# Kernel optimization log

Measured on AMD Instinct MI355X. Metric: run time of the kernel, lower is better.

The kernel has to match this reference:

```python
import jax, jax.numpy as jnp
import numpy as np
import math

D_MODEL = 768
H = 12
D_K = D_MODEL // H


def setup_inputs() -> dict:
    key = jax.random.key(0)
    ks = jax.random.split(key, 12)
    B, S = 2, 2048
    q = jax.random.normal(ks[0], (B, S, D_MODEL), dtype=jnp.float32)
    k = jax.random.normal(ks[1], (B, S, D_MODEL), dtype=jnp.float32)
    v = jax.random.normal(ks[2], (B, S, D_MODEL), dtype=jnp.float32)
    mask = jax.random.randint(ks[3], (1, 1, S, S), 0, 2, dtype=jnp.int32)
    scale = 1.0 / math.sqrt(D_MODEL)
    w_q = jax.random.normal(ks[4], (D_MODEL, D_MODEL), dtype=jnp.float32) * scale
    b_q = jnp.zeros((D_MODEL,), dtype=jnp.float32)
    w_k = jax.random.normal(ks[5], (D_MODEL, D_MODEL), dtype=jnp.float32) * scale
    b_k = jnp.zeros((D_MODEL,), dtype=jnp.float32)
    w_v = jax.random.normal(ks[6], (D_MODEL, D_MODEL), dtype=jnp.float32) * scale
    b_v = jnp.zeros((D_MODEL,), dtype=jnp.float32)
    w_o = jax.random.normal(ks[7], (D_MODEL, D_MODEL), dtype=jnp.float32) * scale
    b_o = jnp.zeros((D_MODEL,), dtype=jnp.float32)
    return {"q": q, "k": k, "v": v, "mask": mask,
            "w_q": w_q, "b_q": b_q, "w_k": w_k, "b_k": b_k,
            "w_v": w_v, "b_v": b_v, "w_o": w_o, "b_o": b_o}


def reference(q, k, v, mask, w_q, b_q, w_k, b_k, w_v, b_v, w_o, b_o):
    B, S, _ = q.shape
    # torch nn.Linear: y = x @ W^T + b
    qp = (q @ w_q.T + b_q).reshape(B, S, H, D_K).transpose(0, 2, 1, 3)  # [B,H,S,Dk]
    kp = (k @ w_k.T + b_k).reshape(B, S, H, D_K).transpose(0, 2, 1, 3)
    vp = (v @ w_v.T + b_v).reshape(B, S, H, D_K).transpose(0, 2, 1, 3)
    # full [B,H,S,S] score matrix (the memory-bound round-trip)
    scores = jnp.einsum('bhqd,bhkd->bhqk', qp, kp) / math.sqrt(D_K)
    scores = jnp.where(mask == 0, jnp.float32(-1e9), scores)
    attn = jax.nn.softmax(scores, axis=-1)
    x = jnp.einsum('bhqk,bhkd->bhqd', attn, vp)  # [B,H,S,Dk]
    x = x.transpose(0, 2, 1, 3).reshape(B, S, H * D_K)
    return x @ w_o.T + b_o
```

## Files before the change

kernel.cpp:

```cpp
#include <hip/hip_runtime.h>
#include <hip/hip_bf16.h>

typedef __attribute__((ext_vector_type(8))) __bf16 bf16x8;
typedef __attribute__((ext_vector_type(8))) short short8;
typedef __attribute__((ext_vector_type(4))) float f32x4;

#define LOG2E 1.44269504088896f
#define SCL (0.125f * 1.44269504088896f)

static __device__ __forceinline__ ushort f2bf(float f) {
  union { float f; unsigned u; } x; x.f = f;
  unsigned r = x.u + 0x7fffu + ((x.u >> 16) & 1u);
  return (ushort)(r >> 16);
}

static __device__ __forceinline__ unsigned cvt_pk_bf16(float a, float b) {
  unsigned r;
  asm("v_cvt_pk_bf16_f32 %0, %1, %2" : "=v"(r) : "v"(a), "v"(b));
  return r;
}

static __device__ __forceinline__ void gll16(const ushort* g, ushort* l) {
  __builtin_amdgcn_global_load_lds(
      (const __attribute__((address_space(1))) unsigned*)g,
      (__attribute__((address_space(3))) unsigned*)l, 16, 0, 0);
}

#define NQ 3145728u
#define NW 589824u
__global__ __launch_bounds__(256)
void cvt_all(const float* __restrict__ q, const float* __restrict__ k,
             const float* __restrict__ v,
             const float* __restrict__ wq, const float* __restrict__ wk,
             const float* __restrict__ wv, const float* __restrict__ wo,
             ushort* __restrict__ dst)
{
  size_t i = ((size_t)blockIdx.x * 256 + threadIdx.x) * 4;
  const float* src; size_t off;
  if (i < NQ)                { src = q;  off = i; }
  else if (i < 2u * NQ)      { src = k;  off = i - NQ; }
  else if (i < 3u * NQ)      { src = v;  off = i - 2u * NQ; }
  else {
    size_t j = i - 3u * NQ;
    if (j < NW)            { src = wq; off = j; }
    else if (j < 2u * NW)  { src = wk; off = j - NW; }
    else if (j < 3u * NW)  { src = wv; off = j - 2u * NW; }
    else                   { src = wo; off = j - 3u * NW; }
  }
  f32x4 x = *(const f32x4*)(src + off);
  uint2 o;
  o.x = cvt_pk_bf16(x[0], x[1]);
  o.y = cvt_pk_bf16(x[2], x[3]);
  *(uint2*)(dst + i) = o;
}

__global__ __launch_bounds__(256)
void mask_pack(const int* __restrict__ mask, unsigned long long* __restrict__ mb)
{
  size_t gw = (size_t)blockIdx.x * 4 + (threadIdx.x >> 6);
  int lane = threadIdx.x & 63;
  int mk = mask[gw * 64 + lane];
  unsigned long long bits = __ballot(mk != 0);
  if (lane == 0) mb[gw] = bits;
}

template<int MODE>
static __device__ __forceinline__ void gemm_core(const ushort* __restrict__ A,
                                                 const ushort* __restrict__ Wrow0,
                                                 const float* __restrict__ bias0,
                                                 void* __restrict__ outv,
                                                 int m0, int c0)
{
  constexpr int K = 768;
  constexpr int BK = 64;
  __shared__ ushort As[2][128 * BK];
  __shared__ ushort Bs[2][128 * BK];
  const int tid  = threadIdx.x;
  const int lane = tid & 63;
  const int wid  = tid >> 6;
  const int wr = (wid >> 1) * 64;
  const int wc = (wid & 1) * 64;

  f32x4 acc[4][4];
#pragma unroll
  for (int i = 0; i < 4; i++)
#pragma unroll
    for (int j = 0; j < 4; j++) acc[i][j] = f32x4{0.f, 0.f, 0.f, 0.f};

  const ushort* gA[4]; const ushort* gB[4];
  int loff[4];
#pragma unroll
  for (int s = 0; s < 4; s++) {
    int idx = tid + s * 256;
    int row = idx >> 3, col = (idx & 7) * 8;
    gA[s] = A     + (size_t)(m0 + row) * K + col;
    gB[s] = Wrow0 + (size_t)row * K + col;
    loff[s] = idx * 8;
  }

  const int fr  = lane & 15;
  const int kg8 = (lane >> 4) * 8;

#pragma unroll
  for (int s = 0; s < 4; s++) {
    gll16(gA[s], &As[0][loff[s]]);
    gll16(gB[s], &Bs[0][loff[s]]);
  }
  __syncthreads();

  int cur = 0;
  for (int t = 0; t < K / BK; t++) {
    if (t < K / BK - 1) {
      const int kt = (t + 1) * BK;
#pragma unroll
      for (int s = 0; s < 4; s++) {
        gll16(gA[s] + kt, &As[cur ^ 1][loff[s]]);
        gll16(gB[s] + kt, &Bs[cur ^ 1][loff[s]]);
      }
    }
    bf16x8 af[2][4], wf[2][4];
#pragma unroll
    for (int kk = 0; kk < 2; kk++) {
#pragma unroll
      for (int i = 0; i < 4; i++) af[kk][i] = *(const bf16x8*)&As[cur][(wr + i * 16 + fr) * BK + kk * 32 + kg8];
#pragma unroll
      for (int j = 0; j < 4; j++) wf[kk][j] = *(const bf16x8*)&Bs[cur][(wc + j * 16 + fr) * BK + kk * 32 + kg8];
    }
#pragma unroll
    for (int kk = 0; kk < 2; kk++)
#pragma unroll
      for (int i = 0; i < 4; i++)
#pragma unroll
        for (int j = 0; j < 4; j++)
          acc[i][j] = __builtin_amdgcn_mfma_f32_16x16x32_bf16(af[kk][i], wf[kk][j], acc[i][j], 0, 0, 0);
    __syncthreads();
    cur ^= 1;
  }

#pragma unroll
  for (int i = 0; i < 4; i++) {
#pragma unroll
    for (int j = 0; j < 4; j++) {
#pragma unroll
      for (int r = 0; r < 4; r++) {
        int m  = m0 + wr + i * 16 + (lane >> 4) * 4 + r;
        int lc = wc + j * 16 + fr;
        float val = acc[i][j][r] + bias0[lc];
        if (MODE == 0) {
          int nn = c0 + lc;
          int hh = nn >> 6, dk = nn & 63;
          ((ushort*)outv)[(((size_t)(m >> 11) * 12 + hh) * 2048 + (m & 2047)) * 64 + dk] = f2bf(val);
        } else {
          ((float*)outv)[(size_t)m * 768 + c0 + lc] = val;
        }
      }
    }
  }
}

__global__ __launch_bounds__(256)
void qkv_gemm2(const ushort* __restrict__ CV,
               const float* __restrict__ bq, const float* __restrict__ bk,
               const float* __restrict__ bv,
               ushort* __restrict__ Qp, ushort* __restrict__ Kp, ushort* __restrict__ Vp)
{
  const int m0 = blockIdx.x * 128;
  const int n0 = blockIdx.y * 128;
  const int proj = n0 / 768;
  const int c0 = n0 - proj * 768;
  const ushort* A  = CV + (size_t)proj * NQ;
  const ushort* Wc = CV + (size_t)3 * NQ;
  const float* bias = (proj == 0) ? bq : (proj == 1) ? bk : bv;
  ushort* O = (proj == 0) ? Qp : (proj == 1) ? Kp : Vp;
  gemm_core<0>(A, Wc + (size_t)n0 * 768, bias + c0, O, m0, c0);
}

__global__ __launch_bounds__(256)
void o_gemm2(const ushort* __restrict__ X, const ushort* __restrict__ Wo,
             const float* __restrict__ bo, float* __restrict__ out)
{
  const int m0 = blockIdx.x * 128;
  const int n0 = blockIdx.y * 128;
  gemm_core<1>(X, Wo + (size_t)n0 * 768, bo + n0, out, m0, n0);
}

__global__ __launch_bounds__(256, 3)
void attn_kernel(const ushort* __restrict__ Qp, const ushort* __restrict__ Kp,
                 const ushort* __restrict__ Vp,
                 const unsigned long long* __restrict__ mb,
                 ushort* __restrict__ X)
{
  constexpr int S = 2048;
  __shared__ ushort Ks[128][72];
  __shared__ ushort Vt[64][136];
  __shared__ ushort Ps[4][16][136];

  const int tid  = threadIdx.x;
  const int lane = tid & 63;
  const int w    = tid >> 6;
  const int bid  = blockIdx.x;
  const int bh = (bid & 7) + 8 * (bid >> 8);
  const int qb = (bid >> 3) & 31;
  const int b = bh / 12, h = bh % 12;

  const ushort* Qb = Qp + (size_t)bh * S * 64;
  const ushort* Kb = Kp + (size_t)bh * S * 64;
  const ushort* Vb = Vp + (size_t)bh * S * 64;

  const int q0  = qb * 64;
  const int fr  = lane & 15;
  const int g   = lane >> 4;
  const int kg8 = g * 8;
  const int qrow4 = q0 + w * 16 + g * 4;

  const int qrow = q0 + w * 16 + fr;
  bf16x8 qf0 = *(const bf16x8*)&Qb[(size_t)qrow * 64 + kg8];
  bf16x8 qf1 = *(const bf16x8*)&Qb[(size_t)qrow * 64 + 32 + kg8];

  float m_r[4] = {-1e9f, -1e9f, -1e9f, -1e9f};
  float l_r[4] = {0.f, 0.f, 0.f, 0.f};
  f32x4 accO[4];
#pragma unroll
  for (int ni = 0; ni < 4; ni++) accO[ni] = f32x4{0.f, 0.f, 0.f, 0.f};

  const int skey = tid >> 2;
  const int sc0  = (tid & 3) * 16;
  const uint4* mb4 = (const uint4*)mb;

  short8 kr0, kr1, kr2, kr3, vr0, vr1, vr2, vr3;
  {
    const ushort* kb = Kb + (size_t)skey * 64 + sc0;
    const ushort* vb = Vb + (size_t)skey * 64 + sc0;
    kr0 = *(const short8*)kb;          kr1 = *(const short8*)(kb + 8);
    kr2 = *(const short8*)(kb + 4096); kr3 = *(const short8*)(kb + 4104);
    vr0 = *(const short8*)vb;          vr1 = *(const short8*)(vb + 8);
    vr2 = *(const short8*)(vb + 4096); vr3 = *(const short8*)(vb + 4104);
  }

  for (int tt = 0; tt < 16; tt++) {
    __syncthreads();
    *(short8*)&Ks[skey][sc0]          = kr0;
    *(short8*)&Ks[skey][sc0 + 8]      = kr1;
    *(short8*)&Ks[64 + skey][sc0]     = kr2;
    *(short8*)&Ks[64 + skey][sc0 + 8] = kr3;
#pragma unroll
    for (int i = 0; i < 8; i++) {
      Vt[sc0 + i][skey]          = (ushort)vr0[i];
      Vt[sc0 + 8 + i][skey]      = (ushort)vr1[i];
      Vt[sc0 + i][64 + skey]     = (ushort)vr2[i];
      Vt[sc0 + 8 + i][64 + skey] = (ushort)vr3[i];
    }
    __syncthreads();

    uint4 mB[4];
#pragma unroll
    for (int r = 0; r < 4; r++)
      mB[r] = mb4[(size_t)(qrow4 + r) * 16 + tt];

    if (tt < 15) {
      const ushort* kb = Kb + (size_t)((tt + 1) * 128 + skey) * 64 + sc0;
      const ushort* vb = Vb + (size_t)((tt + 1) * 128 + skey) * 64 + sc0;
      kr0 = *(const short8*)kb;          kr1 = *(const short8*)(kb + 8);
      kr2 = *(const short8*)(kb + 4096); kr3 = *(const short8*)(kb + 4104);
      vr0 = *(const short8*)vb;          vr1 = *(const short8*)(vb + 8);
      vr2 = *(const short8*)(vb + 4096); vr3 = *(const short8*)(vb + 4104);
    }

    f32x4 sc8[8];
#pragma unroll
    for (int ni = 0; ni < 8; ni++) {
      bf16x8 kf0 = *(const bf16x8*)&Ks[ni * 16 + fr][kg8];
      bf16x8 kf1 = *(const bf16x8*)&Ks[ni * 16 + fr][32 + kg8];
      f32x4 c = {0.f, 0.f, 0.f, 0.f};
      c = __builtin_amdgcn_mfma_f32_16x16x32_bf16(qf0, kf0, c, 0, 0, 0);
      c = __builtin_amdgcn_mfma_f32_16x16x32_bf16(qf1, kf1, c, 0, 0, 0);
      sc8[ni] = c;
    }

#pragma unroll
    for (int r = 0; r < 4; r++) {
      float praw[8];
#pragma unroll
      for (int ni = 0; ni < 8; ni++) praw[ni] = sc8[ni][r] * SCL;
      float mx = fmaxf(fmaxf(fmaxf(praw[0], praw[1]), fmaxf(praw[2], praw[3])),
                       fmaxf(fmaxf(praw[4], praw[5]), fmaxf(praw[6], praw[7])));
      mx = fmaxf(mx, __shfl_xor(mx, 1));
      mx = fmaxf(mx, __shfl_xor(mx, 2));
      mx = fmaxf(mx, __shfl_xor(mx, 4));
      mx = fmaxf(mx, __shfl_xor(mx, 8));
      if (mx > m_r[r] + 11.5f) {
        float al = exp2f(m_r[r] - mx);
        m_r[r] = mx;
        l_r[r] *= al;
#pragma unroll
        for (int ni = 0; ni < 4; ni++) accO[ni][r] *= al;
      }
      const float mr = m_r[r];
      unsigned sx = mB[r].x >> fr, sy = mB[r].y >> fr,
               sz = mB[r].z >> fr, sw = mB[r].w >> fr;
      unsigned bits[8] = { sx & 1u, (sx >> 16) & 1u, sy & 1u, (sy >> 16) & 1u,
                           sz & 1u, (sz >> 16) & 1u, sw & 1u, (sw >> 16) & 1u };
      float e[8];
      float ls = 0.f;
#pragma unroll
      for (int ni = 0; ni < 8; ni++) {
        float t = exp2f(praw[ni] - mr);
        t = bits[ni] ? t : 0.f;
        e[ni] = t; ls += t;
      }
      ls += __shfl_xor(ls, 1);
      ls += __shfl_xor(ls, 2);
      ls += __shfl_xor(ls, 4);
      ls += __shfl_xor(ls, 8);
      l_r[r] += ls;
#pragma unroll
      for (int a = 0; a < 4; a++) {
        unsigned pk = cvt_pk_bf16(e[2 * a], e[2 * a + 1]);
        Ps[w][g * 4 + r][a * 32 + fr]      = (ushort)pk;
        Ps[w][g * 4 + r][a * 32 + 16 + fr] = (ushort)(pk >> 16);
      }
    }

#pragma unroll
    for (int ks = 0; ks < 4; ks++) {
      bf16x8 pf = *(const bf16x8*)&Ps[w][fr][ks * 32 + kg8];
#pragma unroll
      for (int ni = 0; ni < 4; ni++) {
        bf16x8 vf = *(const bf16x8*)&Vt[ni * 16 + fr][ks * 32 + kg8];
        accO[ni] = __builtin_amdgcn_mfma_f32_16x16x32_bf16(pf, vf, accO[ni], 0, 0, 0);
      }
    }
  }

  float inv[4];
#pragma unroll
  for (int r = 0; r < 4; r++) inv[r] = 1.f / l_r[r];
#pragma unroll
  for (int ni = 0; ni < 4; ni++) {
#pragma unroll
    for (int r = 0; r < 4; r++) {
      int qq = qrow4 + r;
      float o = accO[ni][r] * inv[r];
      X[((size_t)b * S + qq) * 768 + h * 64 + ni * 16 + fr] = f2bf(o);
    }
  }
}

extern "C" void kernel_launch(void* const* d_in, const int* in_sizes, int n_in,
                              void* d_out, int out_size, void* d_ws, size_t ws_size,
                              hipStream_t stream) {
  const float* q  = (const float*)d_in[0];
  const float* k  = (const float*)d_in[1];
  const float* v  = (const float*)d_in[2];
  const int* mask = (const int*)d_in[3];
  const float* wq = (const float*)d_in[4];
  const float* bq = (const float*)d_in[5];
  const float* wk = (const float*)d_in[6];
  const float* bk = (const float*)d_in[7];
  const float* wv = (const float*)d_in[8];
  const float* bv = (const float*)d_in[9];
  const float* wo = (const float*)d_in[10];
  const float* bo = (const float*)d_in[11];
  float* out = (float*)d_out;

  ushort* CV = (ushort*)d_ws;
  ushort* Qp = CV + (size_t)3 * NQ + (size_t)4 * NW;
  ushort* Kp = Qp + NQ;
  ushort* Vp = Kp + NQ;
  ushort* Xb = Vp + NQ;
  unsigned long long* mbuf = (unsigned long long*)CV;

  cvt_all<<<11520, 256, 0, stream>>>(q, k, v, wq, wk, wv, wo, CV);
  qkv_gemm2<<<dim3(32, 18), dim3(256), 0, stream>>>(CV, bq, bk, bv, Qp, Kp, Vp);
  mask_pack<<<16384, 256, 0, stream>>>(mask, mbuf);
  attn_kernel<<<768, 256, 0, stream>>>(Qp, Kp, Vp, mbuf, Xb);
  o_gemm2<<<dim3(32, 6), dim3(256), 0, stream>>>(Xb, CV + (size_t)3 * NQ + (size_t)3 * NW, bo, out);
}
```

Before: 266.1 us.

## Store V transposed from QKV GEMM and XOR-swizzle attention LDS tiles

The QKV projection now writes V in a [bh][dk][seq] transposed layout, so the attention kernel can load V^T tiles with vector loads and write them to LDS as 16-byte stores instead of scalar transposing writes. The K, V^T and P shared-memory tiles drop their padding and use an XOR swizzle on the column index to avoid bank conflicts. The aim is to cut LDS store instruction count and bank conflicts in the attention inner loop. In exchange, the GEMM epilogue for V writes with a strided, uncoalesced pattern, which may slow that kernel.

```diff
diff --git a/kernel.cpp b/kernel.cpp
--- a/kernel.cpp
+++ b/kernel.cpp
@@ -150,6 +150,11 @@
           int nn = c0 + lc;
           int hh = nn >> 6, dk = nn & 63;
           ((ushort*)outv)[(((size_t)(m >> 11) * 12 + hh) * 2048 + (m & 2047)) * 64 + dk] = f2bf(val);
+        } else if (MODE == 2) {
+          int nn = c0 + lc;
+          int hh = nn >> 6, dk = nn & 63;
+          int bh = (m >> 11) * 12 + hh;
+          ((ushort*)outv)[((size_t)bh * 64 + dk) * 2048 + (m & 2047)] = f2bf(val);
         } else {
           ((float*)outv)[(size_t)m * 768 + c0 + lc] = val;
         }
@@ -172,7 +177,10 @@
   const ushort* Wc = CV + (size_t)3 * NQ;
   const float* bias = (proj == 0) ? bq : (proj == 1) ? bk : bv;
   ushort* O = (proj == 0) ? Qp : (proj == 1) ? Kp : Vp;
-  gemm_core<0>(A, Wc + (size_t)n0 * 768, bias + c0, O, m0, c0);
+  if (proj == 2)
+    gemm_core<2>(A, Wc + (size_t)n0 * 768, bias + c0, O, m0, c0);
+  else
+    gemm_core<0>(A, Wc + (size_t)n0 * 768, bias + c0, O, m0, c0);
 }
 
 __global__ __launch_bounds__(256)
@@ -186,14 +194,14 @@
 
 __global__ __launch_bounds__(256, 3)
 void attn_kernel(const ushort* __restrict__ Qp, const ushort* __restrict__ Kp,
-                 const ushort* __restrict__ Vp,
+                 const ushort* __restrict__ VpT,
                  const unsigned long long* __restrict__ mb,
                  ushort* __restrict__ X)
 {
   constexpr int S = 2048;
-  __shared__ ushort Ks[128][72];
-  __shared__ ushort Vt[64][136];
-  __shared__ ushort Ps[4][16][136];
+  __shared__ ushort Ks[128][64];
+  __shared__ ushort Vt[64][128];
+  __shared__ ushort Ps[4][16][128];
 
   const int tid  = threadIdx.x;
   const int lane = tid & 63;
@@ -203,9 +211,9 @@
   const int qb = (bid >> 3) & 31;
   const int b = bh / 12, h = bh % 12;
 
-  const ushort* Qb = Qp + (size_t)bh * S * 64;
-  const ushort* Kb = Kp + (size_t)bh * S * 64;
-  const ushort* Vb = Vp + (size_t)bh * S * 64;
+  const ushort* Qb  = Qp  + (size_t)bh * S * 64;
+  const ushort* Kb  = Kp  + (size_t)bh * S * 64;
+  const ushort* gVt = VpT + (size_t)bh * 64 * S;
 
   const int q0  = qb * 64;
   const int fr  = lane & 15;
@@ -225,31 +233,35 @@
 
   const int skey = tid >> 2;
   const int sc0  = (tid & 3) * 16;
+  const int kxor = (skey & 7) << 3;
+  const int vd   = tid >> 4;
+  const int vkc  = (tid & 15) * 8;
+  const int vxor = (vd & 7) << 3;
+
   const uint4* mb4 = (const uint4*)mb;
 
   short8 kr0, kr1, kr2, kr3, vr0, vr1, vr2, vr3;
   {
     const ushort* kb = Kb + (size_t)skey * 64 + sc0;
-    const ushort* vb = Vb + (size_t)skey * 64 + sc0;
     kr0 = *(const short8*)kb;          kr1 = *(const short8*)(kb + 8);
     kr2 = *(const short8*)(kb + 4096); kr3 = *(const short8*)(kb + 4104);
-    vr0 = *(const short8*)vb;          vr1 = *(const short8*)(vb + 8);
-    vr2 = *(const short8*)(vb + 4096); vr3 = *(const short8*)(vb + 4104);
+    const ushort* vb = gVt + (size_t)vd * S + vkc;
+    vr0 = *(const short8*)vb;
+    vr1 = *(const short8*)(vb + 16 * S);
+    vr2 = *(const short8*)(vb + 32 * S);
+    vr3 = *(const short8*)(vb + 48 * S);
   }
 
   for (int tt = 0; tt < 16; tt++) {
     __syncthreads();
-    *(short8*)&Ks[skey][sc0]          = kr0;
-    *(short8*)&Ks[skey][sc0 + 8]      = kr1;
-    *(short8*)&Ks[64 + skey][sc0]     = kr2;
-    *(short8*)&Ks[64 + skey][sc0 + 8] = kr3;
-#pragma unroll
-    for (int i = 0; i < 8; i++) {
-      Vt[sc0 + i][skey]          = (ushort)vr0[i];
-      Vt[sc0 + 8 + i][skey]      = (ushort)vr1[i];
-      Vt[sc0 + i][64 + skey]     = (ushort)vr2[i];
-      Vt[sc0 + 8 + i][64 + skey] = (ushort)vr3[i];
-    }
+    *(short8*)&Ks[skey][sc0 ^ kxor]            = kr0;
+    *(short8*)&Ks[skey][(sc0 + 8) ^ kxor]      = kr1;
+    *(short8*)&Ks[64 + skey][sc0 ^ kxor]       = kr2;
+    *(short8*)&Ks[64 + skey][(sc0 + 8) ^ kxor] = kr3;
+    *(short8*)&Vt[vd][vkc ^ vxor]       = vr0;
+    *(short8*)&Vt[vd + 16][vkc ^ vxor]  = vr1;
+    *(short8*)&Vt[vd + 32][vkc ^ vxor]  = vr2;
+    *(short8*)&Vt[vd + 48][vkc ^ vxor]  = vr3;
     __syncthreads();
 
     uint4 mB[4];
@@ -259,18 +271,22 @@
 
     if (tt < 15) {
       const ushort* kb = Kb + (size_t)((tt + 1) * 128 + skey) * 64 + sc0;
-      const ushort* vb = Vb + (size_t)((tt + 1) * 128 + skey) * 64 + sc0;
       kr0 = *(const short8*)kb;          kr1 = *(const short8*)(kb + 8);
       kr2 = *(const short8*)(kb + 4096); kr3 = *(const short8*)(kb + 4104);
-      vr0 = *(const short8*)vb;          vr1 = *(const short8*)(vb + 8);
-      vr2 = *(const short8*)(vb + 4096); vr3 = *(const short8*)(vb + 4104);
+      const ushort* vb = gVt + (size_t)vd * S + (tt + 1) * 128 + vkc;
+      vr0 = *(const short8*)vb;
+      vr1 = *(const short8*)(vb + 16 * S);
+      vr2 = *(const short8*)(vb + 32 * S);
+      vr3 = *(const short8*)(vb + 48 * S);
     }
 
     f32x4 sc8[8];
 #pragma unroll
     for (int ni = 0; ni < 8; ni++) {
-      bf16x8 kf0 = *(const bf16x8*)&Ks[ni * 16 + fr][kg8];
-      bf16x8 kf1 = *(const bf16x8*)&Ks[ni * 16 + fr][32 + kg8];
+      const int row = ni * 16 + fr;
+      const int rx = (row & 7) << 3;
+      bf16x8 kf0 = *(const bf16x8*)&Ks[row][kg8 ^ rx];
+      bf16x8 kf1 = *(const bf16x8*)&Ks[row][(32 + kg8) ^ rx];
       f32x4 c = {0.f, 0.f, 0.f, 0.f};
       c = __builtin_amdgcn_mfma_f32_16x16x32_bf16(qf0, kf0, c, 0, 0, 0);
       c = __builtin_amdgcn_mfma_f32_16x16x32_bf16(qf1, kf1, c, 0, 0, 0);
@@ -313,20 +329,24 @@
       ls += __shfl_xor(ls, 4);
       ls += __shfl_xor(ls, 8);
       l_r[r] += ls;
+      const int prow = g * 4 + r;
+      const int pxor = (prow & 7) << 3;
 #pragma unroll
       for (int a = 0; a < 4; a++) {
         unsigned pk = cvt_pk_bf16(e[2 * a], e[2 * a + 1]);
-        Ps[w][g * 4 + r][a * 32 + fr]      = (ushort)pk;
-        Ps[w][g * 4 + r][a * 32 + 16 + fr] = (ushort)(pk >> 16);
-      }
-    }
-
+        Ps[w][prow][(a * 32 + fr) ^ pxor]      = (ushort)pk;
+        Ps[w][prow][(a * 32 + 16 + fr) ^ pxor] = (ushort)(pk >> 16);
+      }
+    }
+
+    const int fx = (fr & 7) << 3;
 #pragma unroll
     for (int ks = 0; ks < 4; ks++) {
-      bf16x8 pf = *(const bf16x8*)&Ps[w][fr][ks * 32 + kg8];
+      bf16x8 pf = *(const bf16x8*)&Ps[w][fr][(ks * 32 + kg8) ^ fx];
 #pragma unroll
       for (int ni = 0; ni < 4; ni++) {
-        bf16x8 vf = *(const bf16x8*)&Vt[ni * 16 + fr][ks * 32 + kg8];
+        const int row = ni * 16 + fr;
+        bf16x8 vf = *(const bf16x8*)&Vt[row][(ks * 32 + kg8) ^ ((row & 7) << 3)];
         accO[ni] = __builtin_amdgcn_mfma_f32_16x16x32_bf16(pf, vf, accO[ni], 0, 0, 0);
       }
     }
```

New measurement: 338.6 us. 27.2% more time.

## Transpose QK^T MFMA so each lane owns one query row, swizzle LDS

Applied to the files above, without the earlier changes.

Swaps the MFMA operands for the score computation so each lane holds scores for a single query row across 4 keys. Row max and sum then need only in-lane reductions plus two cross-lane shuffles, instead of four shuffles per row times four rows. K and P tiles in shared memory drop their padding in favour of XOR swizzles to avoid bank conflicts, and P is written with vectorized 8-byte stores. The rescale step now uses a wave-level any() and shuffles the alpha factors back into the output layout, and the mask is loaded once per thread.

```diff
diff --git a/kernel.cpp b/kernel.cpp
--- a/kernel.cpp
+++ b/kernel.cpp
@@ -191,9 +191,9 @@
                  ushort* __restrict__ X)
 {
   constexpr int S = 2048;
-  __shared__ ushort Ks[128][72];
+  __shared__ ushort Ks[128][64];
   __shared__ ushort Vt[64][136];
-  __shared__ ushort Ps[4][16][136];
+  __shared__ ushort Ps[4][16][128];
 
   const int tid  = threadIdx.x;
   const int lane = tid & 63;
@@ -210,21 +210,23 @@
   const int q0  = qb * 64;
   const int fr  = lane & 15;
   const int g   = lane >> 4;
+  const int g4  = g * 4;
   const int kg8 = g * 8;
-  const int qrow4 = q0 + w * 16 + g * 4;
+  const int qrow4 = q0 + w * 16 + g4;
 
   const int qrow = q0 + w * 16 + fr;
   bf16x8 qf0 = *(const bf16x8*)&Qb[(size_t)qrow * 64 + kg8];
   bf16x8 qf1 = *(const bf16x8*)&Qb[(size_t)qrow * 64 + 32 + kg8];
 
-  float m_r[4] = {-1e9f, -1e9f, -1e9f, -1e9f};
-  float l_r[4] = {0.f, 0.f, 0.f, 0.f};
+  float m_s = -1e9f;
+  float l_s = 0.f;
   f32x4 accO[4];
 #pragma unroll
   for (int ni = 0; ni < 4; ni++) accO[ni] = f32x4{0.f, 0.f, 0.f, 0.f};
 
   const int skey = tid >> 2;
   const int sc0  = (tid & 3) * 16;
+  const int kxor = (skey & 7) << 3;
   const uint4* mb4 = (const uint4*)mb;
 
   short8 kr0, kr1, kr2, kr3, vr0, vr1, vr2, vr3;
@@ -239,10 +241,10 @@
 
   for (int tt = 0; tt < 16; tt++) {
     __syncthreads();
-    *(short8*)&Ks[skey][sc0]          = kr0;
-    *(short8*)&Ks[skey][sc0 + 8]      = kr1;
-    *(short8*)&Ks[64 + skey][sc0]     = kr2;
-    *(short8*)&Ks[64 + skey][sc0 + 8] = kr3;
+    *(short8*)&Ks[skey][sc0 ^ kxor]            = kr0;
+    *(short8*)&Ks[skey][(sc0 + 8) ^ kxor]      = kr1;
+    *(short8*)&Ks[64 + skey][sc0 ^ kxor]       = kr2;
+    *(short8*)&Ks[64 + skey][(sc0 + 8) ^ kxor] = kr3;
 #pragma unroll
     for (int i = 0; i < 8; i++) {
       Vt[sc0 + i][skey]          = (ushort)vr0[i];
@@ -252,10 +254,8 @@
     }
     __syncthreads();
 
-    uint4 mB[4];
-#pragma unroll
-    for (int r = 0; r < 4; r++)
-      mB[r] = mb4[(size_t)(qrow4 + r) * 16 + tt];
+    uint4 mq = mb4[(size_t)qrow * 16 + tt];
+    unsigned mw[4] = {mq.x, mq.y, mq.z, mq.w};
 
     if (tt < 15) {
       const ushort* kb = Kb + (size_t)((tt + 1) * 128 + skey) * 64 + sc0;
@@ -269,61 +269,81 @@
     f32x4 sc8[8];
 #pragma unroll
     for (int ni = 0; ni < 8; ni++) {
-      bf16x8 kf0 = *(const bf16x8*)&Ks[ni * 16 + fr][kg8];
-      bf16x8 kf1 = *(const bf16x8*)&Ks[ni * 16 + fr][32 + kg8];
+      const int row = ni * 16 + fr;
+      const int rx = (row & 7) << 3;
+      bf16x8 kf0 = *(const bf16x8*)&Ks[row][kg8 ^ rx];
+      bf16x8 kf1 = *(const bf16x8*)&Ks[row][(32 + kg8) ^ rx];
       f32x4 c = {0.f, 0.f, 0.f, 0.f};
-      c = __builtin_amdgcn_mfma_f32_16x16x32_bf16(qf0, kf0, c, 0, 0, 0);
-      c = __builtin_amdgcn_mfma_f32_16x16x32_bf16(qf1, kf1, c, 0, 0, 0);
+      c = __builtin_amdgcn_mfma_f32_16x16x32_bf16(kf0, qf0, c, 0, 0, 0);
+      c = __builtin_amdgcn_mfma_f32_16x16x32_bf16(kf1, qf1, c, 0, 0, 0);
       sc8[ni] = c;
     }
 
-#pragma unroll
-    for (int r = 0; r < 4; r++) {
-      float praw[8];
-#pragma unroll
-      for (int ni = 0; ni < 8; ni++) praw[ni] = sc8[ni][r] * SCL;
-      float mx = fmaxf(fmaxf(fmaxf(praw[0], praw[1]), fmaxf(praw[2], praw[3])),
-                       fmaxf(fmaxf(praw[4], praw[5]), fmaxf(praw[6], praw[7])));
-      mx = fmaxf(mx, __shfl_xor(mx, 1));
-      mx = fmaxf(mx, __shfl_xor(mx, 2));
-      mx = fmaxf(mx, __shfl_xor(mx, 4));
-      mx = fmaxf(mx, __shfl_xor(mx, 8));
-      if (mx > m_r[r] + 11.5f) {
-        float al = exp2f(m_r[r] - mx);
-        m_r[r] = mx;
-        l_r[r] *= al;
-#pragma unroll
-        for (int ni = 0; ni < 4; ni++) accO[ni][r] *= al;
-      }
-      const float mr = m_r[r];
-      unsigned sx = mB[r].x >> fr, sy = mB[r].y >> fr,
-               sz = mB[r].z >> fr, sw = mB[r].w >> fr;
-      unsigned bits[8] = { sx & 1u, (sx >> 16) & 1u, sy & 1u, (sy >> 16) & 1u,
-                           sz & 1u, (sz >> 16) & 1u, sw & 1u, (sw >> 16) & 1u };
-      float e[8];
-      float ls = 0.f;
-#pragma unroll
-      for (int ni = 0; ni < 8; ni++) {
-        float t = exp2f(praw[ni] - mr);
-        t = bits[ni] ? t : 0.f;
-        e[ni] = t; ls += t;
-      }
-      ls += __shfl_xor(ls, 1);
-      ls += __shfl_xor(ls, 2);
-      ls += __shfl_xor(ls, 4);
-      ls += __shfl_xor(ls, 8);
-      l_r[r] += ls;
-#pragma unroll
-      for (int a = 0; a < 4; a++) {
-        unsigned pk = cvt_pk_bf16(e[2 * a], e[2 * a + 1]);
-        Ps[w][g * 4 + r][a * 32 + fr]      = (ushort)pk;
-        Ps[w][g * 4 + r][a * 32 + 16 + fr] = (ushort)(pk >> 16);
-      }
+    float p[32];
+#pragma unroll
+    for (int ni = 0; ni < 8; ni++)
+#pragma unroll
+      for (int r = 0; r < 4; r++) p[ni * 4 + r] = sc8[ni][r] * SCL;
+
+    float t16[16];
+#pragma unroll
+    for (int z = 0; z < 16; z++) t16[z] = fmaxf(p[z], p[z + 16]);
+#pragma unroll
+    for (int z = 0; z < 8; z++) t16[z] = fmaxf(t16[z], t16[z + 8]);
+#pragma unroll
+    for (int z = 0; z < 4; z++) t16[z] = fmaxf(t16[z], t16[z + 4]);
+    float mx = fmaxf(fmaxf(t16[0], t16[1]), fmaxf(t16[2], t16[3]));
+    mx = fmaxf(mx, __shfl_xor(mx, 16));
+    mx = fmaxf(mx, __shfl_xor(mx, 32));
+
+    bool need = mx > m_s + 11.5f;
+    if (__any(need)) {
+      float mn = need ? mx : m_s;
+      float al = exp2f(m_s - mn);
+      m_s = mn;
+      l_s *= al;
+#pragma unroll
+      for (int r = 0; r < 4; r++) {
+        float alr = __shfl(al, g4 + r);
+#pragma unroll
+        for (int ni = 0; ni < 4; ni++) accO[ni][r] *= alr;
+      }
+    }
+    const float mr = m_s;
+
+#pragma unroll
+    for (int ni = 0; ni < 8; ni++) {
+      unsigned wv = mw[ni >> 1] >> (((ni & 1) * 16) + g4);
+#pragma unroll
+      for (int r = 0; r < 4; r++) {
+        float t = exp2f(p[ni * 4 + r] - mr);
+        p[ni * 4 + r] = ((wv >> r) & 1u) ? t : 0.f;
+      }
+    }
+
+#pragma unroll
+    for (int z = 0; z < 16; z++) t16[z] = p[z] + p[z + 16];
+#pragma unroll
+    for (int z = 0; z < 8; z++) t16[z] += t16[z + 8];
+#pragma unroll
+    for (int z = 0; z < 4; z++) t16[z] += t16[z + 4];
+    float ls = (t16[0] + t16[1]) + (t16[2] + t16[3]);
+    ls += __shfl_xor(ls, 16);
+    ls += __shfl_xor(ls, 32);
+    l_s += ls;
+
+    const int px = (fr & 7) << 3;
+#pragma unroll
+    for (int ni = 0; ni < 8; ni++) {
+      uint2 pk;
+      pk.x = cvt_pk_bf16(p[ni * 4 + 0], p[ni * 4 + 1]);
+      pk.y = cvt_pk_bf16(p[ni * 4 + 2], p[ni * 4 + 3]);
+      *(uint2*)&Ps[w][fr][(ni * 16 + g4) ^ px] = pk;
     }
 
 #pragma unroll
     for (int ks = 0; ks < 4; ks++) {
-      bf16x8 pf = *(const bf16x8*)&Ps[w][fr][ks * 32 + kg8];
+      bf16x8 pf = *(const bf16x8*)&Ps[w][fr][(ks * 32 + kg8) ^ px];
 #pragma unroll
       for (int ni = 0; ni < 4; ni++) {
         bf16x8 vf = *(const bf16x8*)&Vt[ni * 16 + fr][ks * 32 + kg8];
@@ -334,7 +354,7 @@
 
   float inv[4];
 #pragma unroll
-  for (int r = 0; r < 4; r++) inv[r] = 1.f / l_r[r];
+  for (int r = 0; r < 4; r++) inv[r] = 1.f / __shfl(l_s, g4 + r);
 #pragma unroll
   for (int ni = 0; ni < 4; ni++) {
 #pragma unroll
```

Result: faster. 244.6 us (-8.1%).
